# Optimization experiments

Hardware: AMD Instinct MI355X
Metric: run time of the kernel (lower is better)

Reference implementation:

```python
import math
import jax, jax.numpy as jnp
import numpy as np

DIM = 128          # dim == block_size (pow2), n_subblocks == 1, no padding
BITS = 8
N_PASSES = 1
EPS = 1e-8
FINAL_SCALE = DIM ** (-N_PASSES / 2.0)  # makes signed-WHT orthonormal


def _hadamard(n):
    H = np.array([[1.0]], dtype=np.float64)
    while H.shape[0] < n:
        H = np.block([[H, H], [H, -H]])
    return H


def _lloyd_max_gaussian(bits, iters=500):
    """1-D Lloyd-Max quantizer for N(0,1): centroids + inner boundaries."""
    n = 2 ** bits
    phi = lambda t: np.exp(-t * t / 2.0) / math.sqrt(2.0 * math.pi)
    Phi = np.vectorize(lambda t: 0.5 * (1.0 + math.erf(t / math.sqrt(2.0))))
    c = np.linspace(-4.0, 4.0, n)
    for _ in range(iters):
        b = 0.5 * (c[:-1] + c[1:])
        bl = np.concatenate([[-np.inf], b])
        bu = np.concatenate([b, [np.inf]])
        c = (phi(bl) - phi(bu)) / np.maximum(Phi(bu) - Phi(bl), 1e-30)
    bounds = 0.5 * (c[:-1] + c[1:])  # (n-1,) inner decision boundaries
    return c.astype(np.float32), bounds.astype(np.float32)


def setup_inputs() -> dict:
    key = jax.random.key(0)
    kx, ks = jax.random.split(key)
    x = jax.random.normal(kx, (2, 16, 4096, 128), dtype=jnp.float32)
    # Rademacher signs per rotation pass (TurboQuantRotation.all_signs)
    signs = (jax.random.randint(ks, (N_PASSES, DIM), 0, 2) * 2 - 1).astype(jnp.float32)
    wht = jnp.asarray(_hadamard(DIM), dtype=jnp.float32)
    centroids_np, bounds_np = _lloyd_max_gaussian(BITS)
    return {
        "x": x,
        "signs": signs,
        "wht": wht,
        "boundaries": jnp.asarray(bounds_np),
        "centroids": jnp.asarray(centroids_np),
    }


def _rotate(x, signs, wht):
    for p in range(N_PASSES):
        x = (x * signs[p]) @ wht
    return x * FINAL_SCALE


def _rotate_inv(y, signs, wht):
    y = y * FINAL_SCALE
    for p in range(N_PASSES - 1, -1, -1):
        y = (y @ wht.T) * signs[p]
    return y


def reference(x, signs, wht, boundaries, centroids):
    shp = x.shape
    xf = x.reshape(-1, DIM)                                      # [N, 128]
    # --- quantize (CPU fallback path, N > 32 => two-pass gamma refine) ---
    norms = jnp.linalg.norm(xf, axis=-1, keepdims=True) + EPS    # [N, 1]
    x_rot = _rotate(xf / norms, signs, wht)                       # [N, 128]
    max_c = centroids[-1]
    x_max = jnp.max(jnp.abs(x_rot), axis=-1, keepdims=True)
    rms_scales = x_max / max_c
    x_norm = x_rot / (rms_scales + EPS)
    idx_tmp = jnp.searchsorted(boundaries, x_norm)                # bucketize
    recon_u = centroids[idx_tmp]
    num = jnp.sum(x_rot * recon_u, axis=-1, keepdims=True)
    den = jnp.sum(recon_u * recon_u, axis=-1, keepdims=True) + EPS
    gamma1 = num / den
    idx2 = jnp.searchsorted(boundaries, x_rot / (gamma1 + EPS))
    x_mean = jnp.mean(jnp.abs(x_rot), axis=-1, keepdims=True) + EPS
    is_spiky = (x_max / x_mean) > 5.0
    gamma = jnp.where(is_spiky, rms_scales, gamma1)
    idx = jnp.where(is_spiky, idx_tmp, idx2)
    # --- dequantize ---
    recon = centroids[idx] * gamma                                # [N, 128]
    x_unit = _rotate_inv(recon, signs, wht)
    x_hat = x_unit * norms
    return x_hat.reshape(shp)
```

## Files before the change

### kernel.cpp

```cpp
#include <hip/hip_runtime.h>
#include <hip/hip_fp16.h>

#define NCELL 512
#define EPSF  1e-8f
#define FSCD  0.08838834764831845

typedef float f32x2 __attribute__((ext_vector_type(2)));

template<int CTRL>
__device__ __forceinline__ int idpp(int x){
  return __builtin_amdgcn_update_dpp(x, x, CTRL, 0xF, 0xF, false);
}
template<int CTRL>
__device__ __forceinline__ float fdpp(float x){
  return __int_as_float(idpp<CTRL>(__float_as_int(x)));
}
__device__ __forceinline__ float xorl1(float v){ return fdpp<0xB1>(v); }
__device__ __forceinline__ float xorl2(float v){ return fdpp<0x4E>(v); }
__device__ __forceinline__ float xorl4(float v){ return fdpp<0x1B>(fdpp<0x141>(v)); }
__device__ __forceinline__ float xorl8(float v){ return fdpp<0x128>(v); }
template<int CTRL>
__device__ __forceinline__ f32x2 vdpp(f32x2 v){
  f32x2 r; r.x = fdpp<CTRL>(v.x); r.y = fdpp<CTRL>(v.y); return r;
}
__device__ __forceinline__ f32x2 vxor1(f32x2 v){ return vdpp<0xB1>(v); }
__device__ __forceinline__ f32x2 vxor2(f32x2 v){ return vdpp<0x4E>(v); }
__device__ __forceinline__ f32x2 vxor4(f32x2 v){ return vdpp<0x1B>(vdpp<0x141>(v)); }
__device__ __forceinline__ f32x2 vxor8(f32x2 v){ return vdpp<0x128>(v); }

__device__ __forceinline__ float redsum16f(float v){
  v += xorl1(v); v += xorl2(v); v += xorl4(v); v += xorl8(v); return v;
}
__device__ __forceinline__ float redmax16f(float v){
  v = fmaxf(v,xorl1(v)); v = fmaxf(v,xorl2(v));
  v = fmaxf(v,xorl4(v)); v = fmaxf(v,xorl8(v)); return v;
}

__device__ __forceinline__ void fwht128v(f32x2 v[4], f32x2 sA, f32x2 sB,
                                         f32x2 sC, f32x2 sD){
  #pragma unroll
  for (int i = 0; i < 4; ++i) {
    float a = v[i].x, b = v[i].y;
    v[i].x = a + b; v[i].y = a - b;
  }
  { f32x2 t = v[0]; v[0] = t + v[1]; v[1] = t - v[1];
    t = v[2]; v[2] = t + v[3]; v[3] = t - v[3]; }
  { f32x2 t = v[0]; v[0] = t + v[2]; v[2] = t - v[2];
    t = v[1]; v[1] = t + v[3]; v[3] = t - v[3]; }
  #pragma unroll
  for (int i = 0; i < 4; ++i) { f32x2 o = vxor1(v[i]); v[i] = __builtin_elementwise_fma(sA, v[i], o); }
  #pragma unroll
  for (int i = 0; i < 4; ++i) { f32x2 o = vxor2(v[i]); v[i] = __builtin_elementwise_fma(sB, v[i], o); }
  #pragma unroll
  for (int i = 0; i < 4; ++i) { f32x2 o = vxor4(v[i]); v[i] = __builtin_elementwise_fma(sC, v[i], o); }
  #pragma unroll
  for (int i = 0; i < 4; ++i) { f32x2 o = vxor8(v[i]); v[i] = __builtin_elementwise_fma(sD, v[i], o); }
}

__global__ __launch_bounds__(256) void tq_kernel(
    const float* __restrict__ x, const float* __restrict__ signs,
    const float* __restrict__ bnd, const float* __restrict__ ctr,
    float* __restrict__ out, int nquads)
{
  __shared__ uint2  lutE[NCELL];
  __shared__ double Bd[256];
  const int tid = threadIdx.x;
  if (tid < 255)  Bd[tid] = (double)bnd[tid];
  if (tid == 255) Bd[255] = __builtin_inf();
  __syncthreads();

  const double lo    = Bd[0] - 0.01;
  const double cw    = (Bd[254] + 0.01 - lo) * (1.0 / NCELL);
  const double scale = 1.0 / cw;
  const double nls   = -lo * scale;
  const double epsg  = cw * 1e-3;

  for (int c = tid; c < NCELL; c += 256) {
    double wl = (c == 0)         ? -__builtin_inf() : fma((double)c,     cw, lo) - epsg;
    double wr = (c == NCELL - 1) ?  __builtin_inf() : fma((double)(c+1), cw, lo) + epsg;
    int n = 0;
    #pragma unroll
    for (int s = 128; s; s >>= 1) n += (Bd[n + s - 1] < wl) ? s : 0;
    double b  = Bd[n];
    bool  has = (b < wr);
    float c_lo = ctr[n];
    float c_hi = ctr[has ? (n + 1) : n];
    uint2 e;
    e.x = __float_as_uint(has ? (float)b : __builtin_inff());
    e.y = ((unsigned)__half_as_ushort(__float2half_rn(c_hi)) << 16)
        |  (unsigned)__half_as_ushort(__float2half_rn(c_lo));
    lutE[c] = e;
  }
  __syncthreads();

  const int l   = tid & 63;
  const int li  = l & 15;
  const int rw  = (l >> 4) & 3;
  const int wid = tid >> 6;
  const float sAs = (l & 1) ? -1.f : 1.f;
  const float sBs = (l & 2) ? -1.f : 1.f;
  const float sCs = (l & 4) ? -1.f : 1.f;
  const float sDs = (l & 8) ? -1.f : 1.f;
  const f32x2 sAv = { sAs, sAs }, sBv = { sBs, sBs },
              sCv = { sCs, sCs }, sDv = { sDs, sDs };
  const float inv_maxcf = (float)(1.0 / (double)ctr[255]);
  const float scf   = (float)scale;
  const float nlsf  = (float)nls;
  const float icmax = (float)(NCELL - 1);
  const float fscf  = (float)FSCD;

  const float4 sga = *reinterpret_cast<const float4*>(signs + 8 * li);
  const float4 sgb = *reinterpret_cast<const float4*>(signs + 8 * li + 4);
  const f32x2 sg[4] = { { sga.x, sga.y }, { sga.z, sga.w },
                        { sgb.x, sgb.y }, { sgb.z, sgb.w } };

  auto qcent = [&](float vf) -> float {
    float cf = fmaf(vf, scf, nlsf);
    cf = fminf(fmaxf(cf, 0.0f), icmax);
    int ic = (int)cf;
    uint2 e = lutE[ic];
    unsigned h = (__uint_as_float(e.x) < vf) ? (e.y >> 16) : (e.y & 0xFFFFu);
    return __half2float(__ushort_as_half((unsigned short)h));
  };

  const int stride = gridDim.x * 4;
  int t = blockIdx.x * 4 + wid;
  if (t >= nquads) return;

  const int base_off = rw * 128 + 8 * li;
  const float* xp = x + 4 * t * 128 + base_off;
  float4 xa = *reinterpret_cast<const float4*>(xp);
  float4 xb = *reinterpret_cast<const float4*>(xp + 4);

  while (true) {
    const int tn = t + stride;
    const bool more = (tn < nquads);
    const int tpf = more ? tn : t;
    const float* np_ = x + 4 * tpf * 128 + base_off;
    float4 na = *reinterpret_cast<const float4*>(np_);
    float4 nb = *reinterpret_cast<const float4*>(np_ + 4);

    f32x2 r[4];
    r[0] = f32x2{ xa.x, xa.y } * sg[0];
    r[1] = f32x2{ xa.z, xa.w } * sg[1];
    r[2] = f32x2{ xb.x, xb.y } * sg[2];
    r[3] = f32x2{ xb.z, xb.w } * sg[3];

    fwht128v(r, sAv, sBv, sCv, sDv);

    f32x2 ssv = r[0] * r[0];
    f32x2 abv = __builtin_elementwise_abs(r[0]);
    f32x2 mxv = abv, asv = abv;
    #pragma unroll
    for (int i = 1; i < 4; ++i) {
      ssv = __builtin_elementwise_fma(r[i], r[i], ssv);
      f32x2 a = __builtin_elementwise_abs(r[i]);
      mxv = __builtin_elementwise_max(mxv, a);
      asv = asv + a;
    }
    float ssf = ssv.x + ssv.y;
    float mxf = fmaxf(mxv.x, mxv.y);
    float asf = asv.x + asv.y;

    float nf = __builtin_amdgcn_sqrtf(redsum16f(ssf)) * fscf + EPSF;
    float kf = fscf * __builtin_amdgcn_rcpf(nf);

    float xmaxf  = redmax16f(mxf) * kf;
    float xmeanf = fmaf(redsum16f(asf) * 0.0078125f, kf, EPSF);
    bool  spiky  = xmaxf > 5.0f * xmeanf;
    float rmsf   = xmaxf * inv_maxcf;

    float kd1f = kf * __builtin_amdgcn_rcpf(rmsf + EPSF);
    f32x2 c1[4];
    #pragma unroll
    for (int i = 0; i < 4; ++i) {
      c1[i].x = qcent(r[i].x * kd1f);
      c1[i].y = qcent(r[i].y * kd1f);
    }

    f32x2 nmv = r[0] * c1[0];
    f32x2 dnv = c1[0] * c1[0];
    #pragma unroll
    for (int i = 1; i < 4; ++i) {
      nmv = __builtin_elementwise_fma(r[i],  c1[i], nmv);
      dnv = __builtin_elementwise_fma(c1[i], c1[i], dnv);
    }
    float gamma1 = redsum16f(nmv.x + nmv.y) * kf *
                   __builtin_amdgcn_rcpf(redsum16f(dnv.x + dnv.y) + EPSF);

    float kd2f = kf * __builtin_amdgcn_rcpf(gamma1 + EPSF);
    f32x2 c2[4];
    #pragma unroll
    for (int i = 0; i < 4; ++i) {
      c2[i].x = qcent(r[i].x * kd2f);
      c2[i].y = qcent(r[i].y * kd2f);
    }

    float g2s = (spiky ? rmsf : gamma1) * fscf * nf;
    const f32x2 g2v = { g2s, g2s };
    f32x2 y[4];
    #pragma unroll
    for (int i = 0; i < 4; ++i) y[i] = (spiky ? c1[i] : c2[i]) * g2v;
    fwht128v(y, sAv, sBv, sCv, sDv);

    #pragma unroll
    for (int i = 0; i < 4; ++i) y[i] = y[i] * sg[i];
    float4 oa, ob;
    oa.x = y[0].x; oa.y = y[0].y; oa.z = y[1].x; oa.w = y[1].y;
    ob.x = y[2].x; ob.y = y[2].y; ob.z = y[3].x; ob.w = y[3].y;
    float* op = out + 4 * t * 128 + base_off;
    *reinterpret_cast<float4*>(op)     = oa;
    *reinterpret_cast<float4*>(op + 4) = ob;

    if (!more) break;
    t = tn; xa = na; xb = nb;
  }
}

extern "C" void kernel_launch(void* const* d_in, const int* in_sizes, int n_in,
                              void* d_out, int out_size, void* d_ws, size_t ws_size,
                              hipStream_t stream) {
  const float* x     = (const float*)d_in[0];
  const float* signs = (const float*)d_in[1];
  const float* bnd   = (const float*)d_in[3];
  const float* ctr   = (const float*)d_in[4];
  float* out = (float*)d_out;

  int nrows  = out_size / 128;
  int nquads = nrows / 4;
  int blocks = (nquads + 3) / 4;
  if (blocks > 2048) blocks = 2048;
  hipLaunchKernelGGL(tq_kernel, dim3(blocks), dim3(256), 0, stream,
                     x, signs, bnd, ctr, out, nquads);
}
```

Baseline: 39.06 us.

## Build LUT by boundary scatter and launch one quad per wave

Replaces the per-cell binary search over a shared double boundary array with a scatter in which each thread owns one quantizer interval and fills the LUT cells it covers. This removes one __syncthreads and the shared double table. It also drops the persistent grid-stride loop and the 2048-block cap, so every wave handles exactly one group of 4 rows. The cost is that each block now rebuilds the LUT for only 512 rows of work (N = 131072 rows gives 256 quads/... i.e. 8192 blocks), which multiplies setup overhead, and the software prefetch of the next tile is lost.

```diff
diff --git a/kernel.cpp b/kernel.cpp
--- a/kernel.cpp
+++ b/kernel.cpp
@@ -62,34 +62,33 @@
     const float* __restrict__ bnd, const float* __restrict__ ctr,
     float* __restrict__ out, int nquads)
 {
-  __shared__ uint2  lutE[NCELL];
-  __shared__ double Bd[256];
+  __shared__ uint2 lutE[NCELL];
   const int tid = threadIdx.x;
-  if (tid < 255)  Bd[tid] = (double)bnd[tid];
-  if (tid == 255) Bd[255] = __builtin_inf();
-  __syncthreads();
-
-  const double lo    = Bd[0] - 0.01;
-  const double cw    = (Bd[254] + 0.01 - lo) * (1.0 / NCELL);
+
+  const double lo    = (double)bnd[0] - 0.01;
+  const double cw    = ((double)bnd[254] + 0.01 - lo) * (1.0 / NCELL);
   const double scale = 1.0 / cw;
-  const double nls   = -lo * scale;
   const double epsg  = cw * 1e-3;
 
-  for (int c = tid; c < NCELL; c += 256) {
-    double wl = (c == 0)         ? -__builtin_inf() : fma((double)c,     cw, lo) - epsg;
-    double wr = (c == NCELL - 1) ?  __builtin_inf() : fma((double)(c+1), cw, lo) + epsg;
-    int n = 0;
-    #pragma unroll
-    for (int s = 128; s; s >>= 1) n += (Bd[n + s - 1] < wl) ? s : 0;
-    double b  = Bd[n];
-    bool  has = (b < wr);
-    float c_lo = ctr[n];
-    float c_hi = ctr[has ? (n + 1) : n];
-    uint2 e;
-    e.x = __float_as_uint(has ? (float)b : __builtin_inff());
-    e.y = ((unsigned)__half_as_ushort(__float2half_rn(c_hi)) << 16)
-        |  (unsigned)__half_as_ushort(__float2half_rn(c_lo));
-    lutE[c] = e;
+  {
+    const int i = tid;
+    double Bm1 = (i == 0)   ? -__builtin_inf() : (double)bnd[i - 1];
+    double B0  = (i == 255) ?  __builtin_inf() : (double)bnd[i];
+    float  ci  = ctr[i];
+    float  cip = ctr[(i == 255) ? 255 : (i + 1)];
+    int cs = (i == 0)   ? 0     : (int)floor((Bm1 - lo + epsg) * scale) + 1;
+    int ce = (i == 255) ? NCELL : (int)floor((B0  - lo + epsg) * scale) + 1;
+    cs = max(cs, 0); ce = min(ce, NCELL);
+    for (int c = cs; c < ce; ++c) {
+      double wr = (c == NCELL - 1) ? __builtin_inf()
+                                   : fma((double)(c + 1), cw, lo) + epsg;
+      bool has = (B0 < wr);
+      uint2 e;
+      e.x = __float_as_uint(has ? (float)B0 : __builtin_inff());
+      e.y = ((unsigned)__half_as_ushort(__float2half_rn(has ? cip : ci)) << 16)
+          |  (unsigned)__half_as_ushort(__float2half_rn(ci));
+      lutE[c] = e;
+    }
   }
   __syncthreads();
 
@@ -97,15 +96,18 @@
   const int li  = l & 15;
   const int rw  = (l >> 4) & 3;
   const int wid = tid >> 6;
+  const int t   = blockIdx.x * 4 + wid;
+  if (t >= nquads) return;
+
   const float sAs = (l & 1) ? -1.f : 1.f;
   const float sBs = (l & 2) ? -1.f : 1.f;
   const float sCs = (l & 4) ? -1.f : 1.f;
   const float sDs = (l & 8) ? -1.f : 1.f;
   const f32x2 sAv = { sAs, sAs }, sBv = { sBs, sBs },
               sCv = { sCs, sCs }, sDv = { sDs, sDs };
-  const float inv_maxcf = (float)(1.0 / (double)ctr[255]);
+  const float inv_maxcf = 1.0f / ctr[255];
   const float scf   = (float)scale;
-  const float nlsf  = (float)nls;
+  const float nlsf  = (float)(-lo * scale);
   const float icmax = (float)(NCELL - 1);
   const float fscf  = (float)FSCD;
 
@@ -123,98 +125,82 @@
     return __half2float(__ushort_as_half((unsigned short)h));
   };
 
-  const int stride = gridDim.x * 4;
-  int t = blockIdx.x * 4 + wid;
-  if (t >= nquads) return;
-
   const int base_off = rw * 128 + 8 * li;
   const float* xp = x + 4 * t * 128 + base_off;
   float4 xa = *reinterpret_cast<const float4*>(xp);
   float4 xb = *reinterpret_cast<const float4*>(xp + 4);
 
-  while (true) {
-    const int tn = t + stride;
-    const bool more = (tn < nquads);
-    const int tpf = more ? tn : t;
-    const float* np_ = x + 4 * tpf * 128 + base_off;
-    float4 na = *reinterpret_cast<const float4*>(np_);
-    float4 nb = *reinterpret_cast<const float4*>(np_ + 4);
-
-    f32x2 r[4];
-    r[0] = f32x2{ xa.x, xa.y } * sg[0];
-    r[1] = f32x2{ xa.z, xa.w } * sg[1];
-    r[2] = f32x2{ xb.x, xb.y } * sg[2];
-    r[3] = f32x2{ xb.z, xb.w } * sg[3];
-
-    fwht128v(r, sAv, sBv, sCv, sDv);
-
-    f32x2 ssv = r[0] * r[0];
-    f32x2 abv = __builtin_elementwise_abs(r[0]);
-    f32x2 mxv = abv, asv = abv;
-    #pragma unroll
-    for (int i = 1; i < 4; ++i) {
-      ssv = __builtin_elementwise_fma(r[i], r[i], ssv);
-      f32x2 a = __builtin_elementwise_abs(r[i]);
-      mxv = __builtin_elementwise_max(mxv, a);
-      asv = asv + a;
-    }
-    float ssf = ssv.x + ssv.y;
-    float mxf = fmaxf(mxv.x, mxv.y);
-    float asf = asv.x + asv.y;
-
-    float nf = __builtin_amdgcn_sqrtf(redsum16f(ssf)) * fscf + EPSF;
-    float kf = fscf * __builtin_amdgcn_rcpf(nf);
-
-    float xmaxf  = redmax16f(mxf) * kf;
-    float xmeanf = fmaf(redsum16f(asf) * 0.0078125f, kf, EPSF);
-    bool  spiky  = xmaxf > 5.0f * xmeanf;
-    float rmsf   = xmaxf * inv_maxcf;
-
-    float kd1f = kf * __builtin_amdgcn_rcpf(rmsf + EPSF);
-    f32x2 c1[4];
-    #pragma unroll
-    for (int i = 0; i < 4; ++i) {
-      c1[i].x = qcent(r[i].x * kd1f);
-      c1[i].y = qcent(r[i].y * kd1f);
-    }
-
-    f32x2 nmv = r[0] * c1[0];
-    f32x2 dnv = c1[0] * c1[0];
-    #pragma unroll
-    for (int i = 1; i < 4; ++i) {
-      nmv = __builtin_elementwise_fma(r[i],  c1[i], nmv);
-      dnv = __builtin_elementwise_fma(c1[i], c1[i], dnv);
-    }
-    float gamma1 = redsum16f(nmv.x + nmv.y) * kf *
-                   __builtin_amdgcn_rcpf(redsum16f(dnv.x + dnv.y) + EPSF);
-
-    float kd2f = kf * __builtin_amdgcn_rcpf(gamma1 + EPSF);
-    f32x2 c2[4];
-    #pragma unroll
-    for (int i = 0; i < 4; ++i) {
-      c2[i].x = qcent(r[i].x * kd2f);
-      c2[i].y = qcent(r[i].y * kd2f);
-    }
-
-    float g2s = (spiky ? rmsf : gamma1) * fscf * nf;
-    const f32x2 g2v = { g2s, g2s };
-    f32x2 y[4];
-    #pragma unroll
-    for (int i = 0; i < 4; ++i) y[i] = (spiky ? c1[i] : c2[i]) * g2v;
-    fwht128v(y, sAv, sBv, sCv, sDv);
-
-    #pragma unroll
-    for (int i = 0; i < 4; ++i) y[i] = y[i] * sg[i];
-    float4 oa, ob;
-    oa.x = y[0].x; oa.y = y[0].y; oa.z = y[1].x; oa.w = y[1].y;
-    ob.x = y[2].x; ob.y = y[2].y; ob.z = y[3].x; ob.w = y[3].y;
-    float* op = out + 4 * t * 128 + base_off;
-    *reinterpret_cast<float4*>(op)     = oa;
-    *reinterpret_cast<float4*>(op + 4) = ob;
-
-    if (!more) break;
-    t = tn; xa = na; xb = nb;
-  }
+  f32x2 r[4];
+  r[0] = f32x2{ xa.x, xa.y } * sg[0];
+  r[1] = f32x2{ xa.z, xa.w } * sg[1];
+  r[2] = f32x2{ xb.x, xb.y } * sg[2];
+  r[3] = f32x2{ xb.z, xb.w } * sg[3];
+
+  fwht128v(r, sAv, sBv, sCv, sDv);
+
+  f32x2 ssv = r[0] * r[0];
+  f32x2 abv = __builtin_elementwise_abs(r[0]);
+  f32x2 mxv = abv, asv = abv;
+  #pragma unroll
+  for (int i = 1; i < 4; ++i) {
+    ssv = __builtin_elementwise_fma(r[i], r[i], ssv);
+    f32x2 a = __builtin_elementwise_abs(r[i]);
+    mxv = __builtin_elementwise_max(mxv, a);
+    asv = asv + a;
+  }
+  float ssf = ssv.x + ssv.y;
+  float mxf = fmaxf(mxv.x, mxv.y);
+  float asf = asv.x + asv.y;
+
+  float nf = __builtin_amdgcn_sqrtf(redsum16f(ssf)) * fscf + EPSF;
+  float kf = fscf * __builtin_amdgcn_rcpf(nf);
+
+  float xmaxf  = redmax16f(mxf) * kf;
+  float xmeanf = fmaf(redsum16f(asf) * 0.0078125f, kf, EPSF);
+  bool  spiky  = xmaxf > 5.0f * xmeanf;
+  float rmsf   = xmaxf * inv_maxcf;
+
+  float kd1f = kf * __builtin_amdgcn_rcpf(rmsf + EPSF);
+  f32x2 c1[4];
+  #pragma unroll
+  for (int i = 0; i < 4; ++i) {
+    c1[i].x = qcent(r[i].x * kd1f);
+    c1[i].y = qcent(r[i].y * kd1f);
+  }
+
+  f32x2 nmv = r[0] * c1[0];
+  f32x2 dnv = c1[0] * c1[0];
+  #pragma unroll
+  for (int i = 1; i < 4; ++i) {
+    nmv = __builtin_elementwise_fma(r[i],  c1[i], nmv);
+    dnv = __builtin_elementwise_fma(c1[i], c1[i], dnv);
+  }
+  float gamma1 = redsum16f(nmv.x + nmv.y) * kf *
+                 __builtin_amdgcn_rcpf(redsum16f(dnv.x + dnv.y) + EPSF);
+
+  float kd2f = kf * __builtin_amdgcn_rcpf(gamma1 + EPSF);
+  f32x2 c2[4];
+  #pragma unroll
+  for (int i = 0; i < 4; ++i) {
+    c2[i].x = qcent(r[i].x * kd2f);
+    c2[i].y = qcent(r[i].y * kd2f);
+  }
+
+  float g2s = (spiky ? rmsf : gamma1) * fscf * nf;
+  const f32x2 g2v = { g2s, g2s };
+  f32x2 y[4];
+  #pragma unroll
+  for (int i = 0; i < 4; ++i) y[i] = (spiky ? c1[i] : c2[i]) * g2v;
+  fwht128v(y, sAv, sBv, sCv, sDv);
+
+  #pragma unroll
+  for (int i = 0; i < 4; ++i) y[i] = y[i] * sg[i];
+  float4 oa, ob;
+  oa.x = y[0].x; oa.y = y[0].y; oa.z = y[1].x; oa.w = y[1].y;
+  ob.x = y[2].x; ob.y = y[2].y; ob.z = y[3].x; ob.w = y[3].y;
+  float* op = out + 4 * t * 128 + base_off;
+  *reinterpret_cast<float4*>(op)     = oa;
+  *reinterpret_cast<float4*>(op + 4) = ob;
 }
 
 extern "C" void kernel_launch(void* const* d_in, const int* in_sizes, int n_in,
@@ -229,7 +215,6 @@
   int nrows  = out_size / 128;
   int nquads = nrows / 4;
   int blocks = (nquads + 3) / 4;
-  if (blocks > 2048) blocks = 2048;
   hipLaunchKernelGGL(tq_kernel, dim3(blocks), dim3(256), 0, stream,
                      x, signs, bnd, ctr, out, nquads);
 }
```

Result: slower. 40.73 us (+4.3%).
